# Kernel tuning notes

Hardware: AMD Instinct MI355X
Metric: run time of the kernel (lower is better)

## Reference

```python
import jax, jax.numpy as jnp
import numpy as np

N_QUBITS = 4
N_LAYERS = 2
BATCH = 262144


def _bc(theta, ndim):
    # broadcast per-sample angles [B] against a state slice of given ndim
    t = jnp.asarray(theta)
    if t.ndim == 1:
        t = t.reshape((-1,) + (1,) * (ndim - 1))
    return t


def _apply_ry(state, wire, theta):
    # RY(t) = [[cos(t/2), -sin(t/2)], [sin(t/2), cos(t/2)]]
    a0 = jax.lax.index_in_dim(state, 0, axis=wire + 1, keepdims=False)
    a1 = jax.lax.index_in_dim(state, 1, axis=wire + 1, keepdims=False)
    t = _bc(theta, a0.ndim) * 0.5
    c = jnp.cos(t).astype(state.dtype)
    s = jnp.sin(t).astype(state.dtype)
    return jnp.stack([c * a0 - s * a1, s * a0 + c * a1], axis=wire + 1)


def _apply_rz(state, wire, theta):
    # RZ(t) = diag(exp(-i t/2), exp(+i t/2))
    a0 = jax.lax.index_in_dim(state, 0, axis=wire + 1, keepdims=False)
    a1 = jax.lax.index_in_dim(state, 1, axis=wire + 1, keepdims=False)
    t = _bc(theta, a0.ndim) * 0.5
    p = (jnp.cos(t) - 1j * jnp.sin(t)).astype(state.dtype)  # exp(-i t/2)
    return jnp.stack([p * a0, jnp.conj(p) * a1], axis=wire + 1)


def _cnot(state, control, target):
    s0 = jax.lax.index_in_dim(state, 0, axis=control + 1, keepdims=False)
    s1 = jax.lax.index_in_dim(state, 1, axis=control + 1, keepdims=False)
    # axis of target wire after removing the control axis (batch is axis 0)
    t_ax = target + 1 if target < control else target
    s1 = jnp.flip(s1, axis=t_ax)
    return jnp.stack([s0, s1], axis=control + 1)


def setup_inputs() -> dict:
    key = jax.random.key(0)
    kx, kw = jax.random.split(key)
    x = jax.random.uniform(kx, (BATCH, N_QUBITS), dtype=jnp.float32)
    weights = 0.1 * jax.random.normal(kw, (N_LAYERS, N_QUBITS, 2), dtype=jnp.float32)
    return {"x": x, "weights": weights}


def reference(x, weights):
    B = x.shape[0]
    # |0...0> for every sample: [B, 2, 2, 2, 2] complex64
    state = jnp.zeros((B,) + (2,) * N_QUBITS, dtype=jnp.complex64)
    state = state.at[(slice(None),) + (0,) * N_QUBITS].set(1.0)
    # data encoding: per-sample RY on each wire
    for i in range(N_QUBITS):
        state = _apply_ry(state, i, x[:, i])
    # variational layers (shared angles across the batch)
    for layer in range(N_LAYERS):
        for i in range(N_QUBITS):
            state = _apply_ry(state, i, weights[layer, i, 0])
            state = _apply_rz(state, i, weights[layer, i, 1])
        for i in range(N_QUBITS - 1):
            state = _cnot(state, i, i + 1)
        state = _cnot(state, N_QUBITS - 1, 0)
    # <Z_0> = P(bit0=0) - P(bit0=1)
    probs = (state.real ** 2 + state.imag ** 2).reshape(B, 2, -1)
    expz = jnp.sum(probs[:, 0], axis=-1) - jnp.sum(probs[:, 1], axis=-1)
    return expz[:, None].astype(jnp.float32)
```

## Files before the change

kernel.cpp:

```cpp
#include <hip/hip_runtime.h>
#include <math.h>


__global__ void qc_precompute(const float* __restrict__ w, float* __restrict__ wt) {
    int i = threadIdx.x;
    if (i < 8) {
        float ty = 0.5f * w[i * 2 + 0];
        float tz = 0.5f * w[i * 2 + 1];
        float cy, sy, cz, sz;
        sincosf(ty, &sy, &cy);
        sincosf(tz, &sz, &cz);
        wt[i * 4 + 0] = cy;
        wt[i * 4 + 1] = sy;
        wt[i * 4 + 2] = cz;
        wt[i * 4 + 3] = -sz;
    }
}

template <bool PRE>
__global__ __launch_bounds__(256) void qc_main(const float* __restrict__ x,
                                               const float* __restrict__ wsrc,
                                               float* __restrict__ out, int B) {
    int b = blockIdx.x * blockDim.x + threadIdx.x;
    if (b >= B) return;

    float wt[32];
    if (PRE) {
#pragma unroll
        for (int i = 0; i < 32; ++i) wt[i] = wsrc[i];
    } else {
#pragma unroll
        for (int i = 0; i < 8; ++i) {
            float ty = 0.5f * wsrc[i * 2 + 0];
            float tz = 0.5f * wsrc[i * 2 + 1];
            float cy, sy, cz, sz;
            sincosf(ty, &sy, &cy);
            sincosf(tz, &sz, &cz);
            wt[i * 4 + 0] = cy;
            wt[i * 4 + 1] = sy;
            wt[i * 4 + 2] = cz;
            wt[i * 4 + 3] = -sz;
        }
    }

    float4 xv = reinterpret_cast<const float4*>(x)[b];
    float cx[4], sx[4];
    sincosf(0.5f * xv.x, &sx[0], &cx[0]);
    sincosf(0.5f * xv.y, &sx[1], &cx[1]);
    sincosf(0.5f * xv.z, &sx[2], &cx[2]);
    sincosf(0.5f * xv.w, &sx[3], &cx[3]);

    float ar[16], ai[16];
#pragma unroll
    for (int idx = 0; idx < 16; ++idx) {
        float v = 1.0f;
#pragma unroll
        for (int q = 0; q < 4; ++q) {
            int bit = (idx >> (3 - q)) & 1;
            v *= bit ? sx[q] : cx[q];
        }
        ar[idx] = v;
        ai[idx] = 0.0f;
    }

#pragma unroll
    for (int layer = 0; layer < 2; ++layer) {
#pragma unroll
        for (int q = 0; q < 4; ++q) {
            const int base = (layer * 4 + q) * 4;
            const float cy = wt[base + 0], sy = wt[base + 1];
            const float pr = wt[base + 2], pi = wt[base + 3];
            const int m = 8 >> q;
#pragma unroll
            for (int idx = 0; idx < 16; ++idx) {
                if ((idx & m) == 0) {
                    const int i0 = idx, i1 = idx | m;
                    float a0r = ar[i0], a0i = ai[i0];
                    float a1r = ar[i1], a1i = ai[i1];
                    float n0r = cy * a0r - sy * a1r;
                    float n0i = cy * a0i - sy * a1i;
                    float n1r = sy * a0r + cy * a1r;
                    float n1i = sy * a0i + cy * a1i;
                    ar[i0] = pr * n0r - pi * n0i;
                    ai[i0] = pr * n0i + pi * n0r;
                    ar[i1] = pr * n1r + pi * n1i;
                    ai[i1] = pr * n1i - pi * n1r;
                }
            }
        }
#pragma unroll
        for (int k = 0; k < 4; ++k) {
            const int ctrl = k, tgt = (k + 1) & 3;
            const int cm = 8 >> ctrl, tm = 8 >> tgt;
#pragma unroll
            for (int idx = 0; idx < 16; ++idx) {
                if ((idx & cm) && !(idx & tm)) {
                    const int j = idx | tm;
                    float tr = ar[idx]; ar[idx] = ar[j]; ar[j] = tr;
                    float ti = ai[idx]; ai[idx] = ai[j]; ai[j] = ti;
                }
            }
        }
    }

    float e = 0.0f;
#pragma unroll
    for (int idx = 0; idx < 16; ++idx) {
        float p = ar[idx] * ar[idx] + ai[idx] * ai[idx];
        e += (idx & 8) ? -p : p;
    }
    out[b] = e;
}

extern "C" void kernel_launch(void* const* d_in, const int* in_sizes, int n_in,
                              void* d_out, int out_size, void* d_ws, size_t ws_size,
                              hipStream_t stream) {
    const float* x = (const float*)d_in[0];
    const float* w = (const float*)d_in[1];
    float* out = (float*)d_out;
    const int B = in_sizes[0] / 4;
    const int threads = 256;
    const int blocks = (B + threads - 1) / threads;

    if (ws_size >= 32 * sizeof(float)) {
        float* wt = (float*)d_ws;
        qc_precompute<<<1, 64, 0, stream>>>(w, wt);
        qc_main<true><<<blocks, threads, 0, stream>>>(x, wt, out, B);
    } else {
        qc_main<false><<<blocks, threads, 0, stream>>>(x, w, out, B);
    }
}
```

Before: 65.57 us.

## Drop precompute kernel, use fast __sincosf intrinsics, factor initial product state

Removes the separate precompute launch and has every thread compute the weight trig values itself. All sincosf calls become the __sincosf hardware intrinsic, replacing the accurate library routine with its range reduction. The initial product-state amplitudes are built from two 4-entry partial products. This cuts a kernel launch and the per-thread transcendental cost, at the price of lower trig accuracy and redundant per-thread weight trig.

```diff
diff --git a/kernel.cpp b/kernel.cpp
--- a/kernel.cpp
+++ b/kernel.cpp
@@ -2,64 +2,39 @@
 #include <math.h>
 
 
-__global__ void qc_precompute(const float* __restrict__ w, float* __restrict__ wt) {
-    int i = threadIdx.x;
-    if (i < 8) {
-        float ty = 0.5f * w[i * 2 + 0];
-        float tz = 0.5f * w[i * 2 + 1];
-        float cy, sy, cz, sz;
-        sincosf(ty, &sy, &cy);
-        sincosf(tz, &sz, &cz);
-        wt[i * 4 + 0] = cy;
-        wt[i * 4 + 1] = sy;
-        wt[i * 4 + 2] = cz;
-        wt[i * 4 + 3] = -sz;
-    }
-}
-
-template <bool PRE>
 __global__ __launch_bounds__(256) void qc_main(const float* __restrict__ x,
-                                               const float* __restrict__ wsrc,
+                                               const float* __restrict__ w,
                                                float* __restrict__ out, int B) {
     int b = blockIdx.x * blockDim.x + threadIdx.x;
     if (b >= B) return;
 
-    float wt[32];
-    if (PRE) {
+    float cy[8], sy[8], pr[8], pi[8];
 #pragma unroll
-        for (int i = 0; i < 32; ++i) wt[i] = wsrc[i];
-    } else {
-#pragma unroll
-        for (int i = 0; i < 8; ++i) {
-            float ty = 0.5f * wsrc[i * 2 + 0];
-            float tz = 0.5f * wsrc[i * 2 + 1];
-            float cy, sy, cz, sz;
-            sincosf(ty, &sy, &cy);
-            sincosf(tz, &sz, &cz);
-            wt[i * 4 + 0] = cy;
-            wt[i * 4 + 1] = sy;
-            wt[i * 4 + 2] = cz;
-            wt[i * 4 + 3] = -sz;
-        }
+    for (int i = 0; i < 8; ++i) {
+        float s0, c0, s1, c1;
+        __sincosf(0.5f * w[2 * i + 0], &s0, &c0);
+        __sincosf(0.5f * w[2 * i + 1], &s1, &c1);
+        cy[i] = c0; sy[i] = s0;
+        pr[i] = c1; pi[i] = -s1;
     }
 
     float4 xv = reinterpret_cast<const float4*>(x)[b];
     float cx[4], sx[4];
-    sincosf(0.5f * xv.x, &sx[0], &cx[0]);
-    sincosf(0.5f * xv.y, &sx[1], &cx[1]);
-    sincosf(0.5f * xv.z, &sx[2], &cx[2]);
-    sincosf(0.5f * xv.w, &sx[3], &cx[3]);
+    __sincosf(0.5f * xv.x, &sx[0], &cx[0]);
+    __sincosf(0.5f * xv.y, &sx[1], &cx[1]);
+    __sincosf(0.5f * xv.z, &sx[2], &cx[2]);
+    __sincosf(0.5f * xv.w, &sx[3], &cx[3]);
+
+    float v01[4], v23[4];
+    v01[0] = cx[0] * cx[1]; v01[1] = cx[0] * sx[1];
+    v01[2] = sx[0] * cx[1]; v01[3] = sx[0] * sx[1];
+    v23[0] = cx[2] * cx[3]; v23[1] = cx[2] * sx[3];
+    v23[2] = sx[2] * cx[3]; v23[3] = sx[2] * sx[3];
 
     float ar[16], ai[16];
 #pragma unroll
     for (int idx = 0; idx < 16; ++idx) {
-        float v = 1.0f;
-#pragma unroll
-        for (int q = 0; q < 4; ++q) {
-            int bit = (idx >> (3 - q)) & 1;
-            v *= bit ? sx[q] : cx[q];
-        }
-        ar[idx] = v;
+        ar[idx] = v01[idx >> 2] * v23[idx & 3];
         ai[idx] = 0.0f;
     }
 
@@ -67,9 +42,9 @@
     for (int layer = 0; layer < 2; ++layer) {
 #pragma unroll
         for (int q = 0; q < 4; ++q) {
-            const int base = (layer * 4 + q) * 4;
-            const float cy = wt[base + 0], sy = wt[base + 1];
-            const float pr = wt[base + 2], pi = wt[base + 3];
+            const int g = layer * 4 + q;
+            const float c = cy[g], s = sy[g];
+            const float zr = pr[g], zi = pi[g];
             const int m = 8 >> q;
 #pragma unroll
             for (int idx = 0; idx < 16; ++idx) {
@@ -77,14 +52,14 @@
                     const int i0 = idx, i1 = idx | m;
                     float a0r = ar[i0], a0i = ai[i0];
                     float a1r = ar[i1], a1i = ai[i1];
-                    float n0r = cy * a0r - sy * a1r;
-                    float n0i = cy * a0i - sy * a1i;
-                    float n1r = sy * a0r + cy * a1r;
-                    float n1i = sy * a0i + cy * a1i;
-                    ar[i0] = pr * n0r - pi * n0i;
-                    ai[i0] = pr * n0i + pi * n0r;
-                    ar[i1] = pr * n1r + pi * n1i;
-                    ai[i1] = pr * n1i - pi * n1r;
+                    float n0r = c * a0r - s * a1r;
+                    float n0i = c * a0i - s * a1i;
+                    float n1r = s * a0r + c * a1r;
+                    float n1i = s * a0i + c * a1i;
+                    ar[i0] = zr * n0r - zi * n0i;
+                    ai[i0] = zr * n0i + zi * n0r;
+                    ar[i1] = zr * n1r + zi * n1i;
+                    ai[i1] = zr * n1i - zi * n1r;
                 }
             }
         }
@@ -121,12 +96,5 @@
     const int B = in_sizes[0] / 4;
     const int threads = 256;
     const int blocks = (B + threads - 1) / threads;
-
-    if (ws_size >= 32 * sizeof(float)) {
-        float* wt = (float*)d_ws;
-        qc_precompute<<<1, 64, 0, stream>>>(w, wt);
-        qc_main<true><<<blocks, threads, 0, stream>>>(x, wt, out, B);
-    } else {
-        qc_main<false><<<blocks, threads, 0, stream>>>(x, w, out, B);
-    }
+    qc_main<<<blocks, threads, 0, stream>>>(x, w, out, B);
 }
```

New measurement: 62.76 us. 1.04x faster.
